# Kernel tuning notes

Measured on AMD Instinct MI355X. Metric: run time of the kernel, lower is better.

## Reference

```python
import jax, jax.numpy as jnp
import numpy as np

B, S, D, H = 4, 2048, 512, 16
HD = D // H          # head_dim = 32
ROPE_DIM = HD        # rope_pct = 1.0
NEG = -1e30


def apply_rope(x):
    # x: [B, H, S, HD]; rotate first ROPE_DIM dims, half-split (NeoX) convention
    half = ROPE_DIM // 2
    pos = jnp.arange(S, dtype=jnp.float32)
    inv_freq = 1.0 / (10000.0 ** (jnp.arange(0, ROPE_DIM, 2, dtype=jnp.float32) / ROPE_DIM))
    ang = pos[:, None] * inv_freq[None, :]          # [S, half]
    cos, sin = jnp.cos(ang), jnp.sin(ang)           # broadcast over B,H
    x1 = x[..., :half]
    x2 = x[..., half:ROPE_DIM]
    r1 = x1 * cos - x2 * sin
    r2 = x2 * cos + x1 * sin
    rest = x[..., ROPE_DIM:]
    return jnp.concatenate([r1, r2, rest], axis=-1)


def setup_inputs() -> dict:
    key = jax.random.key(0)
    ks = jax.random.split(key, 7)
    x = jax.random.normal(ks[0], (B, S, D), dtype=jnp.float32)
    # causal mask: True = block (j > i)
    attn_mask = jnp.triu(jnp.ones((S, S), dtype=bool), k=1)
    # padding mask: True = PAD; random lengths in [S//2, S]
    lengths = jax.random.randint(ks[1], (B,), S // 2, S + 1)
    key_padding_mask = jnp.arange(S)[None, :] >= lengths[:, None]
    scale = D ** -0.5
    Wq = jax.random.normal(ks[2], (D, D), dtype=jnp.float32) * scale
    Wk = jax.random.normal(ks[3], (D, D), dtype=jnp.float32) * scale
    Wv = jax.random.normal(ks[4], (D, D), dtype=jnp.float32) * scale
    Wo = jax.random.normal(ks[5], (D, D), dtype=jnp.float32) * scale
    return {"x": x, "attn_mask": attn_mask, "key_padding_mask": key_padding_mask,
            "Wq": Wq, "Wk": Wk, "Wv": Wv, "Wo": Wo}


def reference(x, attn_mask, key_padding_mask, Wq, Wk, Wv, Wo):
    scale = HD ** -0.5
    # nn.Linear: y = x @ W.T
    q = (x @ Wq.T).reshape(B, S, H, HD).transpose(0, 2, 1, 3)  # [B,H,S,HD]
    k = (x @ Wk.T).reshape(B, S, H, HD).transpose(0, 2, 1, 3)
    v = (x @ Wv.T).reshape(B, S, H, HD).transpose(0, 2, 1, 3)
    q = apply_rope(q)
    k = apply_rope(k)
    scores = jnp.einsum('bhid,bhjd->bhij', q, k) * scale       # [B,H,S,S]
    scores = jnp.where(key_padding_mask[:, None, None, :], NEG, scores)
    scores = jnp.where(attn_mask[None, None, :, :], NEG, scores)
    probs = jax.nn.softmax(scores.astype(jnp.float32), axis=-1)
    probs = jnp.nan_to_num(probs, nan=0.0)
    ctx = jnp.einsum('bhij,bhjd->bhid', probs, v)              # [B,H,S,HD]
    ctx = ctx.transpose(0, 2, 1, 3).reshape(B, S, D)
    ctx = jnp.where(key_padding_mask[:, :, None], 0.0, ctx)
    return ctx @ Wo.T
```

## Files before the change

kernel.cpp:

```cpp
#include <hip/hip_runtime.h>
#include <hip/hip_bf16.h>

#define B_ 4
#define S_ 2048
#define D_ 512
#define H_ 16
#define HD_ 32

typedef __bf16 bf16;
typedef __bf16 bf16x4 __attribute__((ext_vector_type(4)));
typedef __bf16 bf16x8 __attribute__((ext_vector_type(8)));
typedef float f32x4 __attribute__((ext_vector_type(4)));

__device__ __forceinline__ f32x4 mfma16(bf16x8 a, bf16x8 b, f32x4 c) {
  return __builtin_amdgcn_mfma_f32_16x16x32_bf16(a, b, c, 0, 0, 0);
}

__device__ __forceinline__ bf16x8 cvt8(const float* __restrict__ p) {
  const f32x4* v = (const f32x4*)p;
  f32x4 a = v[0], b = v[1];
  bf16x8 r;
  r[0] = (bf16)a[0]; r[1] = (bf16)a[1]; r[2] = (bf16)a[2]; r[3] = (bf16)a[3];
  r[4] = (bf16)b[0]; r[5] = (bf16)b[1]; r[6] = (bf16)b[2]; r[7] = (bf16)b[3];
  return r;
}

__global__ __launch_bounds__(256) void prep_kernel(
    const float* __restrict__ x, const float* __restrict__ wq,
    const float* __restrict__ wk, const float* __restrict__ wv,
    const float* __restrict__ wo, const unsigned char* __restrict__ am,
    const unsigned char* __restrict__ kpm, bf16* __restrict__ xb,
    bf16* __restrict__ dq, bf16* __restrict__ dk, bf16* __restrict__ dv,
    bf16* __restrict__ dwo, int* __restrict__ lengths_out) {
  int bid = blockIdx.x;
  if (bid < 2048) {
    size_t i = (size_t)bid * 256 + threadIdx.x;
    *(bf16x8*)(xb + i * 8) = cvt8(x + i * 8);
  } else if (bid < 2560) {
    int wb = bid - 2048;
    int mat = wb >> 7;
    size_t i = (size_t)(wb & 127) * 256 + threadIdx.x;
    const float* s = (mat == 0) ? wq : (mat == 1) ? wk : (mat == 2) ? wv : wo;
    bf16* d = (mat == 0) ? dq : (mat == 1) ? dk : (mat == 2) ? dv : dwo;
    *(bf16x8*)(d + i * 8) = cvt8(s + i * 8);
  } else {
    int b = threadIdx.x >> 6, lane = threadIdx.x & 63;
    int esize;
    if (am[1] == 1) esize = 1;
    else if (am[2] == 0x80 && am[3] == 0x3F) esize = 2;
    else if (am[3] == 0x3C) esize = 2;
    else if (am[4] == 1) esize = 4;
    else if (am[6] == 0x80 && am[7] == 0x3F) esize = 4;
    else if (am[8] == 1) esize = 8;
    else esize = 1;
    int cnt = 0;
    for (int i = lane; i < S_; i += 64) {
      size_t off = ((size_t)b * S_ + i) * (size_t)esize;
      unsigned char nz = 0;
      for (int e = 0; e < esize; ++e) nz |= kpm[off + e];
      cnt += (nz == 0) ? 1 : 0;
    }
    for (int off = 1; off < 64; off <<= 1) cnt += __shfl_xor(cnt, off);
    if (lane == 0) lengths_out[b] = cnt;
  }
}

#define LDK 40

__global__ __launch_bounds__(256) void qkv_rope_kernel(
    const bf16* __restrict__ x,
    const bf16* __restrict__ Wq, const bf16* __restrict__ Wk,
    const bf16* __restrict__ Wv,
    bf16* __restrict__ q_ws,
    bf16* __restrict__ k_ws,
    bf16* __restrict__ vt_ws)
{
  __shared__ __align__(16) bf16 As[2][128 * LDK];
  __shared__ __align__(16) bf16 Bs[2][128 * LDK];

  int bid = blockIdx.x;
  int brow = bid / 12, bc = bid % 12;
  int mat = bc >> 2;
  const bf16* W = (mat == 0) ? Wq : (mat == 1) ? Wk : Wv;
  int row0 = brow * 128;
  int col0 = (bc & 3) * 128;

  int tid = threadIdx.x;
  int w = tid >> 6, l = tid & 63;
  int wr = w >> 1, wc = w & 1;
  int g = l >> 4, c = l & 15;
  int srow = tid >> 2, skg = tid & 3;

  f32x4 acc[4][4];
  f32x4 zero = {0.f, 0.f, 0.f, 0.f};
#pragma unroll
  for (int m = 0; m < 4; ++m)
#pragma unroll
    for (int n = 0; n < 4; ++n) acc[m][n] = zero;

  bf16x8 rA[2], rB[2];
#pragma unroll
  for (int hh = 0; hh < 2; ++hh) {
    int r = hh * 64 + srow;
    rA[hh] = *(const bf16x8*)(x + (size_t)(row0 + r) * 512 + skg * 8);
    rB[hh] = *(const bf16x8*)(W + (size_t)(col0 + r) * 512 + skg * 8);
  }
#pragma unroll
  for (int hh = 0; hh < 2; ++hh) {
    int r = hh * 64 + srow;
    *(bf16x8*)(&As[0][r * LDK + skg * 8]) = rA[hh];
    *(bf16x8*)(&Bs[0][r * LDK + skg * 8]) = rB[hh];
  }
  __syncthreads();
  int cur = 0;

#pragma unroll 1
  for (int k0 = 0; k0 < 512; k0 += 32) {
    bool more = (k0 < 480);
    if (more) {
#pragma unroll
      for (int hh = 0; hh < 2; ++hh) {
        int r = hh * 64 + srow;
        rA[hh] = *(const bf16x8*)(x + (size_t)(row0 + r) * 512 + k0 + 32 + skg * 8);
        rB[hh] = *(const bf16x8*)(W + (size_t)(col0 + r) * 512 + k0 + 32 + skg * 8);
      }
    }
    bf16x8 af[4], bfr[4];
#pragma unroll
    for (int m = 0; m < 4; ++m)
      af[m] = *(const bf16x8*)(&As[cur][(wr * 64 + m * 16 + c) * LDK + g * 8]);
#pragma unroll
    for (int n = 0; n < 4; ++n)
      bfr[n] = *(const bf16x8*)(&Bs[cur][(wc * 64 + n * 16 + c) * LDK + g * 8]);
#pragma unroll
    for (int m = 0; m < 4; ++m)
#pragma unroll
      for (int n = 0; n < 4; ++n) acc[m][n] = mfma16(af[m], bfr[n], acc[m][n]);
    if (more) {
#pragma unroll
      for (int hh = 0; hh < 2; ++hh) {
        int r = hh * 64 + srow;
        *(bf16x8*)(&As[cur ^ 1][r * LDK + skg * 8]) = rA[hh];
        *(bf16x8*)(&Bs[cur ^ 1][r * LDK + skg * 8]) = rB[hh];
      }
      __syncthreads();
      cur ^= 1;
    }
  }

  if (mat < 2) {
    bf16* dst = (mat == 0) ? q_ws : k_ws;
    float invf = powf(10000.0f, -(float)c * (1.0f / 16.0f));
#pragma unroll
    for (int m = 0; m < 4; ++m) {
      int rbase = row0 + wr * 64 + m * 16 + g * 4;
#pragma unroll
      for (int r = 0; r < 4; ++r) {
        int grow = rbase + r;
        int bb = grow >> 11, s = grow & (S_ - 1);
        float ang = (float)s * invf;
        float cs = cosf(ang), sn = sinf(ang);
#pragma unroll
        for (int np = 0; np < 2; ++np) {
          int n = np * 2;
          int obase = col0 + wc * 64 + n * 16;
          int h = obase >> 5;
          float a0 = acc[m][n][r], a1 = acc[m][n + 1][r];
          size_t base = (((size_t)bb * H_ + h) * S_ + s) * HD_;
          dst[base + c] = (bf16)(a0 * cs - a1 * sn);
          dst[base + c + 16] = (bf16)(a1 * cs + a0 * sn);
        }
      }
    }
  } else {
#pragma unroll
    for (int m = 0; m < 4; ++m) {
      int rbase = row0 + wr * 64 + m * 16 + g * 4;
#pragma unroll
      for (int n = 0; n < 4; ++n) {
        int o = col0 + wc * 64 + n * 16 + c;
        int h = o >> 5, hd = o & 31;
#pragma unroll
        for (int r = 0; r < 4; ++r) {
          int grow = rbase + r;
          int bb = grow >> 11, s = grow & (S_ - 1);
          vt_ws[(((size_t)bb * H_ + h) * HD_ + hd) * S_ + s] = (bf16)acc[m][n][r];
        }
      }
    }
  }
}

#define LDK2 40
#define LDV 72
#define LDP 72
__global__ __launch_bounds__(256) void attn_kernel(
    const bf16* __restrict__ q_ws, const bf16* __restrict__ k_ws,
    const bf16* __restrict__ vt_ws, const int* __restrict__ lengths,
    bf16* __restrict__ ctx_ws)
{
  __shared__ __align__(16) bf16 Ks[2][64 * LDK2];
  __shared__ __align__(16) bf16 Vts[2][HD_ * LDV];
  __shared__ __align__(16) bf16 Ps[4][16 * LDP];

  int p = blockIdx.x;
  int bh = blockIdx.y;
  int bb = bh >> 4, h = bh & 15;
  int tid = threadIdx.x, w = tid >> 6, l = tid & 63, g = l >> 4, c = l & 15;
  const size_t bh_base = ((size_t)bb * H_ + h) * (size_t)S_ * HD_;
  const float escale = 0.17677669529663687f * 1.4426950408889634f;
  int len = lengths[bb];
  int rowrel = w * 16 + c;

  int srowK = tid >> 2, skgK = tid & 3;
  int srowV = tid >> 3, ssgV = tid & 7;

#pragma unroll 1
  for (int phase = 0; phase < 2; ++phase) {
    int qt = phase ? (31 - p) : p;
    int q0 = qt * 64 + w * 16;

    bf16x8 qf = *(const bf16x8*)(q_ws + bh_base + (size_t)(q0 + c) * HD_ + g * 8);

    f32x4 zero = {0.f, 0.f, 0.f, 0.f};
    f32x4 ctxa[2];
    ctxa[0] = zero; ctxa[1] = zero;
    float lrun = 0.f;

    bf16x8 regK = *(const bf16x8*)(k_ws + bh_base + (size_t)srowK * HD_ + skgK * 8);
    bf16x8 regV = *(const bf16x8*)(vt_ws + bh_base + (size_t)srowV * S_ + ssgV * 8);
    __syncthreads();
    *(bf16x8*)(&Ks[0][srowK * LDK2 + skgK * 8]) = regK;
    *(bf16x8*)(&Vts[0][srowV * LDV + ssgV * 8]) = regV;
    __syncthreads();
    int cur = 0;

#pragma unroll 1
    for (int kt = 0; kt <= qt; ++kt) {
      bool hasNext = (kt < qt);
      if (hasNext) {
        regK = *(const bf16x8*)(k_ws + bh_base +
                                (size_t)((kt + 1) * 64 + srowK) * HD_ + skgK * 8);
        regV = *(const bf16x8*)(vt_ws + bh_base + (size_t)srowV * S_ +
                                (kt + 1) * 64 + ssgV * 8);
      }
      const bf16* KsC = Ks[cur];
      const bf16* VtsC = Vts[cur];

      f32x4 sacc[4];
#pragma unroll
      for (int n = 0; n < 4; ++n) {
        bf16x8 kf = *(const bf16x8*)(&KsC[(n * 16 + c) * LDK2 + g * 8]);
        sacc[n] = mfma16(kf, qf, zero);
      }

      float sv[4][4];
      if (kt != qt) {
#pragma unroll
        for (int n = 0; n < 4; ++n)
#pragma unroll
          for (int r = 0; r < 4; ++r)
            sv[n][r] = __builtin_amdgcn_exp2f(sacc[n][r] * escale);
      } else {
#pragma unroll
        for (int n = 0; n < 4; ++n) {
          int jr = n * 16 + g * 4;
#pragma unroll
          for (int r = 0; r < 4; ++r) {
            float e = __builtin_amdgcn_exp2f(sacc[n][r] * escale);
            sv[n][r] = (jr + r > rowrel) ? 0.f : e;
          }
        }
      }
#pragma unroll
      for (int n = 0; n < 4; ++n)
        lrun += (sv[n][0] + sv[n][1]) + (sv[n][2] + sv[n][3]);

#pragma unroll
      for (int n = 0; n < 4; ++n) {
        bf16x4 pk;
        pk[0] = (bf16)sv[n][0]; pk[1] = (bf16)sv[n][1];
        pk[2] = (bf16)sv[n][2]; pk[3] = (bf16)sv[n][3];
        *(bf16x4*)(&Ps[w][c * LDP + n * 16 + g * 4]) = pk;
      }

      bf16x8 pf0 = *(const bf16x8*)(&Ps[w][c * LDP + g * 8]);
      bf16x8 pf1 = *(const bf16x8*)(&Ps[w][c * LDP + 32 + g * 8]);
#pragma unroll
      for (int n = 0; n < 2; ++n) {
        bf16x8 v0 = *(const bf16x8*)(&VtsC[(n * 16 + c) * LDV + g * 8]);
        bf16x8 v1 = *(const bf16x8*)(&VtsC[(n * 16 + c) * LDV + 32 + g * 8]);
        ctxa[n] = mfma16(pf0, v0, ctxa[n]);
        ctxa[n] = mfma16(pf1, v1, ctxa[n]);
      }

      if (hasNext) {
        *(bf16x8*)(&Ks[cur ^ 1][srowK * LDK2 + skgK * 8]) = regK;
        *(bf16x8*)(&Vts[cur ^ 1][srowV * LDV + ssgV * 8]) = regV;
        __syncthreads();
        cur ^= 1;
      }
    }

    float tot = lrun + __shfl_xor(lrun, 16);
    tot += __shfl_xor(tot, 32);
    float lr[4];
#pragma unroll
    for (int r = 0; r < 4; ++r) lr[r] = __shfl(tot, g * 4 + r);
#pragma unroll
    for (int n = 0; n < 2; ++n)
#pragma unroll
      for (int r = 0; r < 4; ++r) {
        int qr = q0 + g * 4 + r;
        float val = ctxa[n][r] / lr[r];
        if (qr >= len) val = 0.f;
        ctx_ws[(((size_t)bb * S_ + qr) * H_ + h) * HD_ + n * 16 + c] = (bf16)val;
      }
  }
}

__global__ __launch_bounds__(256) void out_proj_kernel(
    const bf16* __restrict__ ctx, const bf16* __restrict__ Wo,
    float* __restrict__ out) {
  __shared__ __align__(16) bf16 As[2][128 * LDK];
  __shared__ __align__(16) bf16 Bs[2][128 * LDK];

  int bid = blockIdx.x;
  int brow = bid >> 2, bc = bid & 3;
  int row0 = brow * 128, col0 = bc * 128;
  int tid = threadIdx.x;
  int w = tid >> 6, l = tid & 63;
  int wr = w >> 1, wc = w & 1;
  int g = l >> 4, c = l & 15;
  int srow = tid >> 2, skg = tid & 3;

  f32x4 acc[4][4];
  f32x4 zero = {0.f, 0.f, 0.f, 0.f};
#pragma unroll
  for (int m = 0; m < 4; ++m)
#pragma unroll
    for (int n = 0; n < 4; ++n) acc[m][n] = zero;

  bf16x8 rA[2], rB[2];
#pragma unroll
  for (int hh = 0; hh < 2; ++hh) {
    int r = hh * 64 + srow;
    rA[hh] = *(const bf16x8*)(ctx + (size_t)(row0 + r) * 512 + skg * 8);
    rB[hh] = *(const bf16x8*)(Wo + (size_t)(col0 + r) * 512 + skg * 8);
  }
#pragma unroll
  for (int hh = 0; hh < 2; ++hh) {
    int r = hh * 64 + srow;
    *(bf16x8*)(&As[0][r * LDK + skg * 8]) = rA[hh];
    *(bf16x8*)(&Bs[0][r * LDK + skg * 8]) = rB[hh];
  }
  __syncthreads();
  int cur = 0;

#pragma unroll 1
  for (int k0 = 0; k0 < 512; k0 += 32) {
    bool more = (k0 < 480);
    if (more) {
#pragma unroll
      for (int hh = 0; hh < 2; ++hh) {
        int r = hh * 64 + srow;
        rA[hh] = *(const bf16x8*)(ctx + (size_t)(row0 + r) * 512 + k0 + 32 + skg * 8);
        rB[hh] = *(const bf16x8*)(Wo + (size_t)(col0 + r) * 512 + k0 + 32 + skg * 8);
      }
    }
    bf16x8 af[4], bfr[4];
#pragma unroll
    for (int m = 0; m < 4; ++m)
      af[m] = *(const bf16x8*)(&As[cur][(wr * 64 + m * 16 + c) * LDK + g * 8]);
#pragma unroll
    for (int n = 0; n < 4; ++n)
      bfr[n] = *(const bf16x8*)(&Bs[cur][(wc * 64 + n * 16 + c) * LDK + g * 8]);
#pragma unroll
    for (int m = 0; m < 4; ++m)
#pragma unroll
      for (int n = 0; n < 4; ++n) acc[m][n] = mfma16(af[m], bfr[n], acc[m][n]);
    if (more) {
#pragma unroll
      for (int hh = 0; hh < 2; ++hh) {
        int r = hh * 64 + srow;
        *(bf16x8*)(&As[cur ^ 1][r * LDK + skg * 8]) = rA[hh];
        *(bf16x8*)(&Bs[cur ^ 1][r * LDK + skg * 8]) = rB[hh];
      }
      __syncthreads();
      cur ^= 1;
    }
  }

#pragma unroll
  for (int m = 0; m < 4; ++m) {
    int rbase = row0 + wr * 64 + m * 16 + g * 4;
#pragma unroll
    for (int n = 0; n < 4; ++n) {
      int o = col0 + wc * 64 + n * 16 + c;
#pragma unroll
      for (int r = 0; r < 4; ++r)
        out[(size_t)(rbase + r) * 512 + o] = acc[m][n][r];
    }
  }
}

extern "C" void kernel_launch(void* const* d_in, const int* in_sizes, int n_in,
                              void* d_out, int out_size, void* d_ws,
                              size_t ws_size, hipStream_t stream) {
  const float* x = (const float*)d_in[0];
  const unsigned char* am = (const unsigned char*)d_in[1];
  const unsigned char* kpm = (const unsigned char*)d_in[2];
  const float* Wq = (const float*)d_in[3];
  const float* Wk = (const float*)d_in[4];
  const float* Wv = (const float*)d_in[5];
  const float* Wo = (const float*)d_in[6];
  float* out = (float*)d_out;

  char* ws = (char*)d_ws;
  int* lengths = (int*)ws;
  const size_t QKV_ELEMS = (size_t)B_ * H_ * S_ * HD_;
  const size_t W_ELEMS = (size_t)D_ * D_;
  bf16* xb = (bf16*)(ws + 256);
  bf16* q_ws = xb + QKV_ELEMS;
  bf16* k_ws = q_ws + QKV_ELEMS;
  bf16* vt_ws = k_ws + QKV_ELEMS;
  bf16* wqb = vt_ws + QKV_ELEMS;
  bf16* wkb = wqb + W_ELEMS;
  bf16* wvb = wkb + W_ELEMS;
  bf16* wob = wvb + W_ELEMS;
  bf16* ctx_ws = xb;

  hipLaunchKernelGGL(prep_kernel, dim3(2561), dim3(256), 0, stream, x, Wq, Wk,
                     Wv, Wo, am, kpm, xb, wqb, wkb, wvb, wob, lengths);
  hipLaunchKernelGGL(qkv_rope_kernel, dim3(768), dim3(256), 0, stream, xb, wqb,
                     wkb, wvb, q_ws, k_ws, vt_ws);
  hipLaunchKernelGGL(attn_kernel, dim3(16, 64), dim3(256), 0, stream, q_ws, k_ws,
                     vt_ws, lengths, ctx_ws);
  hipLaunchKernelGGL(out_proj_kernel, dim3(256), dim3(256), 0, stream, ctx_ws,
                     wob, out);
}
```

Before: 126.7 us.

## Enlarge attention query tile to 128 rows and stage V-transpose stores through LDS

```diff
diff --git a/kernel.cpp b/kernel.cpp
--- a/kernel.cpp
+++ b/kernel.cpp
@@ -66,6 +66,7 @@
 }
 
 #define LDK 40
+#define LDT 136
 
 __global__ __launch_bounds__(256) void qkv_rope_kernel(
     const bf16* __restrict__ x,
@@ -75,8 +76,10 @@
     bf16* __restrict__ k_ws,
     bf16* __restrict__ vt_ws)
 {
-  __shared__ __align__(16) bf16 As[2][128 * LDK];
-  __shared__ __align__(16) bf16 Bs[2][128 * LDK];
+  __shared__ __align__(16) bf16 smem[20480];
+#define AS(b) (smem + (b) * 5120)
+#define BS(b) (smem + 10240 + (b) * 5120)
+#define CT smem
 
   int bid = blockIdx.x;
   int brow = bid / 12, bc = bid % 12;
@@ -108,8 +111,8 @@
 #pragma unroll
   for (int hh = 0; hh < 2; ++hh) {
     int r = hh * 64 + srow;
-    *(bf16x8*)(&As[0][r * LDK + skg * 8]) = rA[hh];
-    *(bf16x8*)(&Bs[0][r * LDK + skg * 8]) = rB[hh];
+    *(bf16x8*)(&AS(0)[r * LDK + skg * 8]) = rA[hh];
+    *(bf16x8*)(&BS(0)[r * LDK + skg * 8]) = rB[hh];
   }
   __syncthreads();
   int cur = 0;
@@ -128,10 +131,10 @@
     bf16x8 af[4], bfr[4];
 #pragma unroll
     for (int m = 0; m < 4; ++m)
-      af[m] = *(const bf16x8*)(&As[cur][(wr * 64 + m * 16 + c) * LDK + g * 8]);
+      af[m] = *(const bf16x8*)(&AS(cur)[(wr * 64 + m * 16 + c) * LDK + g * 8]);
 #pragma unroll
     for (int n = 0; n < 4; ++n)
-      bfr[n] = *(const bf16x8*)(&Bs[cur][(wc * 64 + n * 16 + c) * LDK + g * 8]);
+      bfr[n] = *(const bf16x8*)(&BS(cur)[(wc * 64 + n * 16 + c) * LDK + g * 8]);
 #pragma unroll
     for (int m = 0; m < 4; ++m)
 #pragma unroll
@@ -140,8 +143,8 @@
 #pragma unroll
       for (int hh = 0; hh < 2; ++hh) {
         int r = hh * 64 + srow;
-        *(bf16x8*)(&As[cur ^ 1][r * LDK + skg * 8]) = rA[hh];
-        *(bf16x8*)(&Bs[cur ^ 1][r * LDK + skg * 8]) = rB[hh];
+        *(bf16x8*)(&AS(cur ^ 1)[r * LDK + skg * 8]) = rA[hh];
+        *(bf16x8*)(&BS(cur ^ 1)[r * LDK + skg * 8]) = rB[hh];
       }
       __syncthreads();
       cur ^= 1;
@@ -173,22 +176,33 @@
       }
     }
   } else {
+    __syncthreads();
 #pragma unroll
     for (int m = 0; m < 4; ++m) {
-      int rbase = row0 + wr * 64 + m * 16 + g * 4;
 #pragma unroll
       for (int n = 0; n < 4; ++n) {
-        int o = col0 + wc * 64 + n * 16 + c;
-        int h = o >> 5, hd = o & 31;
-#pragma unroll
-        for (int r = 0; r < 4; ++r) {
-          int grow = rbase + r;
-          int bb = grow >> 11, s = grow & (S_ - 1);
-          vt_ws[(((size_t)bb * H_ + h) * HD_ + hd) * S_ + s] = (bf16)acc[m][n][r];
-        }
-      }
-    }
-  }
+        int o = wc * 64 + n * 16 + c;
+        int sb = wr * 64 + m * 16 + g * 4;
+        bf16x4 q4;
+        q4[0] = (bf16)acc[m][n][0]; q4[1] = (bf16)acc[m][n][1];
+        q4[2] = (bf16)acc[m][n][2]; q4[3] = (bf16)acc[m][n][3];
+        *(bf16x4*)(&CT[o * LDT + sb]) = q4;
+      }
+    }
+    __syncthreads();
+    int o_l = tid >> 1, sh = (tid & 1) * 64;
+    int o = col0 + o_l;
+    int h = o >> 5, hd = o & 31;
+    int bb2 = row0 >> 11, sr = row0 & (S_ - 1);
+    size_t dst = (((size_t)bb2 * H_ + h) * HD_ + hd) * S_ + sr + sh;
+#pragma unroll
+    for (int j = 0; j < 8; ++j)
+      *(bf16x8*)(vt_ws + dst + j * 8) =
+          *(const bf16x8*)(&CT[o_l * LDT + sh + j * 8]);
+  }
+#undef AS
+#undef BS
+#undef CT
 }
 
 #define LDK2 40
@@ -201,7 +215,7 @@
 {
   __shared__ __align__(16) bf16 Ks[2][64 * LDK2];
   __shared__ __align__(16) bf16 Vts[2][HD_ * LDV];
-  __shared__ __align__(16) bf16 Ps[4][16 * LDP];
+  __shared__ __align__(16) bf16 Ps[4][32 * LDP];
 
   int p = blockIdx.x;
   int bh = blockIdx.y;
@@ -210,22 +224,27 @@
   const size_t bh_base = ((size_t)bb * H_ + h) * (size_t)S_ * HD_;
   const float escale = 0.17677669529663687f * 1.4426950408889634f;
   int len = lengths[bb];
-  int rowrel = w * 16 + c;
 
   int srowK = tid >> 2, skgK = tid & 3;
   int srowV = tid >> 3, ssgV = tid & 7;
 
 #pragma unroll 1
   for (int phase = 0; phase < 2; ++phase) {
-    int qt = phase ? (31 - p) : p;
-    int q0 = qt * 64 + w * 16;
-
-    bf16x8 qf = *(const bf16x8*)(q_ws + bh_base + (size_t)(q0 + c) * HD_ + g * 8);
+    int qt = phase ? (15 - p) : p;
+    int q0 = qt * 128 + w * 32;
+    int ktmax = 2 * qt + 1;
+
+    bf16x8 qf[2];
+#pragma unroll
+    for (int m = 0; m < 2; ++m)
+      qf[m] = *(const bf16x8*)(q_ws + bh_base + (size_t)(q0 + m * 16 + c) * HD_ +
+                               g * 8);
 
     f32x4 zero = {0.f, 0.f, 0.f, 0.f};
-    f32x4 ctxa[2];
-    ctxa[0] = zero; ctxa[1] = zero;
-    float lrun = 0.f;
+    f32x4 ctxa[2][2];
+#pragma unroll
+    for (int m = 0; m < 2; ++m) { ctxa[m][0] = zero; ctxa[m][1] = zero; }
+    float lrun[2] = {0.f, 0.f};
 
     bf16x8 regK = *(const bf16x8*)(k_ws + bh_base + (size_t)srowK * HD_ + skgK * 8);
     bf16x8 regV = *(const bf16x8*)(vt_ws + bh_base + (size_t)srowV * S_ + ssgV * 8);
@@ -236,8 +255,8 @@
     int cur = 0;
 
 #pragma unroll 1
-    for (int kt = 0; kt <= qt; ++kt) {
-      bool hasNext = (kt < qt);
+    for (int kt = 0; kt <= ktmax; ++kt) {
+      bool hasNext = (kt < ktmax);
       if (hasNext) {
         regK = *(const bf16x8*)(k_ws + bh_base +
                                 (size_t)((kt + 1) * 64 + srowK) * HD_ + skgK * 8);
@@ -247,51 +266,70 @@
       const bf16* KsC = Ks[cur];
       const bf16* VtsC = Vts[cur];
 
-      f32x4 sacc[4];
-#pragma unroll
-      for (int n = 0; n < 4; ++n) {
-        bf16x8 kf = *(const bf16x8*)(&KsC[(n * 16 + c) * LDK2 + g * 8]);
-        sacc[n] = mfma16(kf, qf, zero);
-      }
-
-      float sv[4][4];
-      if (kt != qt) {
+      bool dead = (kt * 64 > q0 + 31);
+      if (!dead) {
+        bool diag = (kt >= 2 * qt);
+        bf16x8 kf[4];
 #pragma unroll
         for (int n = 0; n < 4; ++n)
-#pragma unroll
-          for (int r = 0; r < 4; ++r)
-            sv[n][r] = __builtin_amdgcn_exp2f(sacc[n][r] * escale);
-      } else {
-#pragma unroll
-        for (int n = 0; n < 4; ++n) {
-          int jr = n * 16 + g * 4;
-#pragma unroll
-          for (int r = 0; r < 4; ++r) {
-            float e = __builtin_amdgcn_exp2f(sacc[n][r] * escale);
-            sv[n][r] = (jr + r > rowrel) ? 0.f : e;
+          kf[n] = *(const bf16x8*)(&KsC[(n * 16 + c) * LDK2 + g * 8]);
+
+#pragma unroll
+        for (int m = 0; m < 2; ++m) {
+          f32x4 sacc[4];
+#pragma unroll
+          for (int n = 0; n < 4; ++n) sacc[n] = mfma16(kf[n], qf[m], zero);
+
+          float sv[4][4];
+          if (!diag) {
+#pragma unroll
+            for (int n = 0; n < 4; ++n)
+#pragma unroll
+              for (int r = 0; r < 4; ++r)
+                sv[n][r] = __builtin_amdgcn_exp2f(sacc[n][r] * escale);
+          } else {
+            int rowg = q0 + m * 16 + c;
+#pragma unroll
+            for (int n = 0; n < 4; ++n) {
+              int jg = kt * 64 + n * 16 + g * 4;
+#pragma unroll
+              for (int r = 0; r < 4; ++r) {
+                float e = __builtin_amdgcn_exp2f(sacc[n][r] * escale);
+                sv[n][r] = (jg + r > rowg) ? 0.f : e;
+              }
+            }
+          }
+#pragma unroll
+          for (int n = 0; n < 4; ++n)
+            lrun[m] += (sv[n][0] + sv[n][1]) + (sv[n][2] + sv[n][3]);
+
+#pragma unroll
+          for (int n = 0; n < 4; ++n) {
+            bf16x4 pk;
+            pk[0] = (bf16)sv[n][0]; pk[1] = (bf16)sv[n][1];
+            pk[2] = (bf16)sv[n][2]; pk[3] = (bf16)sv[n][3];
+            *(bf16x4*)(&Ps[w][(m * 16 + c) * LDP + n * 16 + g * 4]) = pk;
           }
         }
-      }
-#pragma unroll
-      for (int n = 0; n < 4; ++n)
-        lrun += (sv[n][0] + sv[n][1]) + (sv[n][2] + sv[n][3]);
-
-#pragma unroll
-      for (int n = 0; n < 4; ++n) {
-        bf16x4 pk;
-        pk[0] = (bf16)sv[n][0]; pk[1] = (bf16)sv[n][1];
-        pk[2] = (bf16)sv[n][2]; pk[3] = (bf16)sv[n][3];
-        *(bf16x4*)(&Ps[w][c * LDP + n * 16 + g * 4]) = pk;
-      }
-
-      bf16x8 pf0 = *(const bf16x8*)(&Ps[w][c * LDP + g * 8]);
-      bf16x8 pf1 = *(const bf16x8*)(&Ps[w][c * LDP + 32 + g * 8]);
-#pragma unroll
-      for (int n = 0; n < 2; ++n) {
-        bf16x8 v0 = *(const bf16x8*)(&VtsC[(n * 16 + c) * LDV + g * 8]);
-        bf16x8 v1 = *(const bf16x8*)(&VtsC[(n * 16 + c) * LDV + 32 + g * 8]);
-        ctxa[n] = mfma16(pf0, v0, ctxa[n]);
-        ctxa[n] = mfma16(pf1, v1, ctxa[n]);
+
+        bf16x8 vf[2][2];
+#pragma unroll
+        for (int n2 = 0; n2 < 2; ++n2)
+#pragma unroll
+          for (int kh = 0; kh < 2; ++kh)
+            vf[n2][kh] =
+                *(const bf16x8*)(&VtsC[(n2 * 16 + c) * LDV + kh * 32 + g * 8]);
+#pragma unroll
+        for (int m = 0; m < 2; ++m) {
+#pragma unroll
+          for (int kh = 0; kh < 2; ++kh) {
+            bf16x8 pf =
+                *(const bf16x8*)(&Ps[w][(m * 16 + c) * LDP + kh * 32 + g * 8]);
+#pragma unroll
+            for (int n2 = 0; n2 < 2; ++n2)
+              ctxa[m][n2] = mfma16(pf, vf[n2][kh], ctxa[m][n2]);
+          }
+        }
       }
 
       if (hasNext) {
@@ -302,20 +340,24 @@
       }
     }
 
-    float tot = lrun + __shfl_xor(lrun, 16);
-    tot += __shfl_xor(tot, 32);
-    float lr[4];
-#pragma unroll
-    for (int r = 0; r < 4; ++r) lr[r] = __shfl(tot, g * 4 + r);
-#pragma unroll
-    for (int n = 0; n < 2; ++n)
-#pragma unroll
-      for (int r = 0; r < 4; ++r) {
-        int qr = q0 + g * 4 + r;
-        float val = ctxa[n][r] / lr[r];
-        if (qr >= len) val = 0.f;
-        ctx_ws[(((size_t)bb * S_ + qr) * H_ + h) * HD_ + n * 16 + c] = (bf16)val;
-      }
+#pragma unroll
+    for (int m = 0; m < 2; ++m) {
+      float tot = lrun[m] + __shfl_xor(lrun[m], 16);
+      tot += __shfl_xor(tot, 32);
+      float lr[4];
+#pragma unroll
+      for (int r = 0; r < 4; ++r) lr[r] = __shfl(tot, g * 4 + r);
+#pragma unroll
+      for (int n2 = 0; n2 < 2; ++n2)
+#pragma unroll
+        for (int r = 0; r < 4; ++r) {
+          int qr = q0 + m * 16 + g * 4 + r;
+          float val = ctxa[m][n2][r] / lr[r];
+          if (qr >= len) val = 0.f;
+          ctx_ws[(((size_t)bb * S_ + qr) * H_ + h) * HD_ + n2 * 16 + c] =
+              (bf16)val;
+        }
+    }
   }
 }
 
@@ -434,7 +476,7 @@
                      Wv, Wo, am, kpm, xb, wqb, wkb, wvb, wob, lengths);
   hipLaunchKernelGGL(qkv_rope_kernel, dim3(768), dim3(256), 0, stream, xb, wqb,
                      wkb, wvb, q_ws, k_ws, vt_ws);
-  hipLaunchKernelGGL(attn_kernel, dim3(16, 64), dim3(256), 0, stream, q_ws, k_ws,
+  hipLaunchKernelGGL(attn_kernel, dim3(8, 64), dim3(256), 0, stream, q_ws, k_ws,
                      vt_ws, lengths, ctx_ws);
   hipLaunchKernelGGL(out_proj_kernel, dim3(256), dim3(256), 0, stream, ctx_ws,
                      wob, out);
```

Measured after the change: 133.8 us. 5.6% more time.

## Use direct global-to-LDS loads in projection GEMMs and stage V transpose through LDS

Applied to the files above, without the earlier changes.

```diff
diff --git a/kernel.cpp b/kernel.cpp
--- a/kernel.cpp
+++ b/kernel.cpp
@@ -14,6 +14,12 @@
 
 __device__ __forceinline__ f32x4 mfma16(bf16x8 a, bf16x8 b, f32x4 c) {
   return __builtin_amdgcn_mfma_f32_16x16x32_bf16(a, b, c, 0, 0, 0);
+}
+
+__device__ __forceinline__ void gload16(const bf16* g, bf16* l) {
+  __builtin_amdgcn_global_load_lds(
+      (const __attribute__((address_space(1))) void*)g,
+      (__attribute__((address_space(3))) void*)l, 16, 0, 0);
 }
 
 __device__ __forceinline__ bf16x8 cvt8(const float* __restrict__ p) {
@@ -65,8 +71,7 @@
   }
 }
 
-#define LDK 40
-
+#define LDT 136
 __global__ __launch_bounds__(256) void qkv_rope_kernel(
     const bf16* __restrict__ x,
     const bf16* __restrict__ Wq, const bf16* __restrict__ Wk,
@@ -75,8 +80,10 @@
     bf16* __restrict__ k_ws,
     bf16* __restrict__ vt_ws)
 {
-  __shared__ __align__(16) bf16 As[2][128 * LDK];
-  __shared__ __align__(16) bf16 Bs[2][128 * LDK];
+  __shared__ __align__(16) bf16 smem[17408];
+#define AS(b) (smem + (b) * 4096)
+#define BS(b) (smem + 8192 + (b) * 4096)
+#define CT smem
 
   int bid = blockIdx.x;
   int brow = bid / 12, bc = bid % 12;
@@ -89,7 +96,8 @@
   int w = tid >> 6, l = tid & 63;
   int wr = w >> 1, wc = w & 1;
   int g = l >> 4, c = l & 15;
-  int srow = tid >> 2, skg = tid & 3;
+  int lrow = l >> 2;
+  int lcol = (l & 3) * 8;
 
   f32x4 acc[4][4];
   f32x4 zero = {0.f, 0.f, 0.f, 0.f};
@@ -98,18 +106,12 @@
 #pragma unroll
     for (int n = 0; n < 4; ++n) acc[m][n] = zero;
 
-  bf16x8 rA[2], rB[2];
-#pragma unroll
-  for (int hh = 0; hh < 2; ++hh) {
-    int r = hh * 64 + srow;
-    rA[hh] = *(const bf16x8*)(x + (size_t)(row0 + r) * 512 + skg * 8);
-    rB[hh] = *(const bf16x8*)(W + (size_t)(col0 + r) * 512 + skg * 8);
-  }
-#pragma unroll
-  for (int hh = 0; hh < 2; ++hh) {
-    int r = hh * 64 + srow;
-    *(bf16x8*)(&As[0][r * LDK + skg * 8]) = rA[hh];
-    *(bf16x8*)(&Bs[0][r * LDK + skg * 8]) = rB[hh];
+#pragma unroll
+  for (int j = 0; j < 2; ++j) {
+    int chunk = w * 2 + j;
+    int grow = chunk * 16 + lrow;
+    gload16(x + (size_t)(row0 + grow) * 512 + lcol, AS(0) + chunk * 512);
+    gload16(W + (size_t)(col0 + grow) * 512 + lcol, BS(0) + chunk * 512);
   }
   __syncthreads();
   int cur = 0;
@@ -119,30 +121,27 @@
     bool more = (k0 < 480);
     if (more) {
 #pragma unroll
-      for (int hh = 0; hh < 2; ++hh) {
-        int r = hh * 64 + srow;
-        rA[hh] = *(const bf16x8*)(x + (size_t)(row0 + r) * 512 + k0 + 32 + skg * 8);
-        rB[hh] = *(const bf16x8*)(W + (size_t)(col0 + r) * 512 + k0 + 32 + skg * 8);
+      for (int j = 0; j < 2; ++j) {
+        int chunk = w * 2 + j;
+        int grow = chunk * 16 + lrow;
+        gload16(x + (size_t)(row0 + grow) * 512 + k0 + 32 + lcol,
+                AS(cur ^ 1) + chunk * 512);
+        gload16(W + (size_t)(col0 + grow) * 512 + k0 + 32 + lcol,
+                BS(cur ^ 1) + chunk * 512);
       }
     }
     bf16x8 af[4], bfr[4];
 #pragma unroll
     for (int m = 0; m < 4; ++m)
-      af[m] = *(const bf16x8*)(&As[cur][(wr * 64 + m * 16 + c) * LDK + g * 8]);
+      af[m] = *(const bf16x8*)(AS(cur) + (wr * 64 + m * 16 + c) * 32 + g * 8);
 #pragma unroll
     for (int n = 0; n < 4; ++n)
-      bfr[n] = *(const bf16x8*)(&Bs[cur][(wc * 64 + n * 16 + c) * LDK + g * 8]);
+      bfr[n] = *(const bf16x8*)(BS(cur) + (wc * 64 + n * 16 + c) * 32 + g * 8);
 #pragma unroll
     for (int m = 0; m < 4; ++m)
 #pragma unroll
       for (int n = 0; n < 4; ++n) acc[m][n] = mfma16(af[m], bfr[n], acc[m][n]);
     if (more) {
-#pragma unroll
-      for (int hh = 0; hh < 2; ++hh) {
-        int r = hh * 64 + srow;
-        *(bf16x8*)(&As[cur ^ 1][r * LDK + skg * 8]) = rA[hh];
-        *(bf16x8*)(&Bs[cur ^ 1][r * LDK + skg * 8]) = rB[hh];
-      }
       __syncthreads();
       cur ^= 1;
     }
@@ -173,22 +172,33 @@
       }
     }
   } else {
+    __syncthreads();
 #pragma unroll
     for (int m = 0; m < 4; ++m) {
-      int rbase = row0 + wr * 64 + m * 16 + g * 4;
 #pragma unroll
       for (int n = 0; n < 4; ++n) {
-        int o = col0 + wc * 64 + n * 16 + c;
-        int h = o >> 5, hd = o & 31;
-#pragma unroll
-        for (int r = 0; r < 4; ++r) {
-          int grow = rbase + r;
-          int bb = grow >> 11, s = grow & (S_ - 1);
-          vt_ws[(((size_t)bb * H_ + h) * HD_ + hd) * S_ + s] = (bf16)acc[m][n][r];
-        }
-      }
-    }
-  }
+        int o = wc * 64 + n * 16 + c;
+        int sb = wr * 64 + m * 16 + g * 4;
+        bf16x4 q4;
+        q4[0] = (bf16)acc[m][n][0]; q4[1] = (bf16)acc[m][n][1];
+        q4[2] = (bf16)acc[m][n][2]; q4[3] = (bf16)acc[m][n][3];
+        *(bf16x4*)(&CT[o * LDT + sb]) = q4;
+      }
+    }
+    __syncthreads();
+    int o_l = tid >> 1, sh = (tid & 1) * 64;
+    int o = col0 + o_l;
+    int h = o >> 5, hd = o & 31;
+    int bb2 = row0 >> 11, sr = row0 & (S_ - 1);
+    size_t dst = (((size_t)bb2 * H_ + h) * HD_ + hd) * S_ + sr + sh;
+#pragma unroll
+    for (int j = 0; j < 8; ++j)
+      *(bf16x8*)(vt_ws + dst + j * 8) =
+          *(const bf16x8*)(&CT[o_l * LDT + sh + j * 8]);
+  }
+#undef AS
+#undef BS
+#undef CT
 }
 
 #define LDK2 40
@@ -322,8 +332,8 @@
 __global__ __launch_bounds__(256) void out_proj_kernel(
     const bf16* __restrict__ ctx, const bf16* __restrict__ Wo,
     float* __restrict__ out) {
-  __shared__ __align__(16) bf16 As[2][128 * LDK];
-  __shared__ __align__(16) bf16 Bs[2][128 * LDK];
+  __shared__ __align__(16) bf16 As[2][4096];
+  __shared__ __align__(16) bf16 Bs[2][4096];
 
   int bid = blockIdx.x;
   int brow = bid >> 2, bc = bid & 3;
@@ -332,7 +342,8 @@
   int w = tid >> 6, l = tid & 63;
   int wr = w >> 1, wc = w & 1;
   int g = l >> 4, c = l & 15;
-  int srow = tid >> 2, skg = tid & 3;
+  int lrow = l >> 2;
+  int lcol = (l & 3) * 8;
 
   f32x4 acc[4][4];
   f32x4 zero = {0.f, 0.f, 0.f, 0.f};
@@ -341,18 +352,12 @@
 #pragma unroll
     for (int n = 0; n < 4; ++n) acc[m][n] = zero;
 
-  bf16x8 rA[2], rB[2];
-#pragma unroll
-  for (int hh = 0; hh < 2; ++hh) {
-    int r = hh * 64 + srow;
-    rA[hh] = *(const bf16x8*)(ctx + (size_t)(row0 + r) * 512 + skg * 8);
-    rB[hh] = *(const bf16x8*)(Wo + (size_t)(col0 + r) * 512 + skg * 8);
-  }
-#pragma unroll
-  for (int hh = 0; hh < 2; ++hh) {
-    int r = hh * 64 + srow;
-    *(bf16x8*)(&As[0][r * LDK + skg * 8]) = rA[hh];
-    *(bf16x8*)(&Bs[0][r * LDK + skg * 8]) = rB[hh];
+#pragma unroll
+  for (int j = 0; j < 2; ++j) {
+    int chunk = w * 2 + j;
+    int grow = chunk * 16 + lrow;
+    gload16(ctx + (size_t)(row0 + grow) * 512 + lcol, As[0] + chunk * 512);
+    gload16(Wo + (size_t)(col0 + grow) * 512 + lcol, Bs[0] + chunk * 512);
   }
   __syncthreads();
   int cur = 0;
@@ -362,30 +367,27 @@
     bool more = (k0 < 480);
     if (more) {
 #pragma unroll
-      for (int hh = 0; hh < 2; ++hh) {
-        int r = hh * 64 + srow;
-        rA[hh] = *(const bf16x8*)(ctx + (size_t)(row0 + r) * 512 + k0 + 32 + skg * 8);
-        rB[hh] = *(const bf16x8*)(Wo + (size_t)(col0 + r) * 512 + k0 + 32 + skg * 8);
+      for (int j = 0; j < 2; ++j) {
+        int chunk = w * 2 + j;
+        int grow = chunk * 16 + lrow;
+        gload16(ctx + (size_t)(row0 + grow) * 512 + k0 + 32 + lcol,
+                As[cur ^ 1] + chunk * 512);
+        gload16(Wo + (size_t)(col0 + grow) * 512 + k0 + 32 + lcol,
+                Bs[cur ^ 1] + chunk * 512);
       }
     }
     bf16x8 af[4], bfr[4];
 #pragma unroll
     for (int m = 0; m < 4; ++m)
-      af[m] = *(const bf16x8*)(&As[cur][(wr * 64 + m * 16 + c) * LDK + g * 8]);
+      af[m] = *(const bf16x8*)(As[cur] + (wr * 64 + m * 16 + c) * 32 + g * 8);
 #pragma unroll
     for (int n = 0; n < 4; ++n)
-      bfr[n] = *(const bf16x8*)(&Bs[cur][(wc * 64 + n * 16 + c) * LDK + g * 8]);
+      bfr[n] = *(const bf16x8*)(Bs[cur] + (wc * 64 + n * 16 + c) * 32 + g * 8);
 #pragma unroll
     for (int m = 0; m < 4; ++m)
 #pragma unroll
       for (int n = 0; n < 4; ++n) acc[m][n] = mfma16(af[m], bfr[n], acc[m][n]);
     if (more) {
-#pragma unroll
-      for (int hh = 0; hh < 2; ++hh) {
-        int r = hh * 64 + srow;
-        *(bf16x8*)(&As[cur ^ 1][r * LDK + skg * 8]) = rA[hh];
-        *(bf16x8*)(&Bs[cur ^ 1][r * LDK + skg * 8]) = rB[hh];
-      }
       __syncthreads();
       cur ^= 1;
     }
```

After: 127.1 us. Within noise of the previous version (+0.4%).
